# Performance work log

Measured on AMD Instinct MI355X. Metric: run time of the kernel, lower is better.

## Reference

```python
import jax, jax.numpy as jnp
import numpy as np

D_MODEL = 1024
NUM_HEADS = 16
HEAD_DIM = D_MODEL // NUM_HEADS
BATCH, SEQ = 2, 2048


def setup_inputs() -> dict:
    key = jax.random.key(0)
    ks = jax.random.split(key, 11)
    s = 1.0 / np.sqrt(D_MODEL)
    inp = {
        "query": jax.random.normal(ks[0], (BATCH, SEQ, D_MODEL), jnp.float32),
        "key": jax.random.normal(ks[1], (BATCH, SEQ, D_MODEL), jnp.float32),
        "value": jax.random.normal(ks[2], (BATCH, SEQ, D_MODEL), jnp.float32),
        "q_w": jax.random.uniform(ks[3], (D_MODEL, D_MODEL), jnp.float32, -s, s),
        "q_b": jax.random.uniform(ks[4], (D_MODEL,), jnp.float32, -s, s),
        "k_w": jax.random.uniform(ks[5], (D_MODEL, D_MODEL), jnp.float32, -s, s),
        "k_b": jax.random.uniform(ks[6], (D_MODEL,), jnp.float32, -s, s),
        "v_w": jax.random.uniform(ks[7], (D_MODEL, D_MODEL), jnp.float32, -s, s),
        "v_b": jax.random.uniform(ks[8], (D_MODEL,), jnp.float32, -s, s),
        "o_w": jax.random.uniform(ks[9], (D_MODEL, D_MODEL), jnp.float32, -s, s),
        "o_b": jax.random.uniform(ks[10], (D_MODEL,), jnp.float32, -s, s),
    }
    return inp


def reference(query, key, value, q_w, q_b, k_w, k_b, v_w, v_b, o_w, o_b):
    B = query.shape[0]
    # linear projections (torch Linear: x @ W^T + b)
    q = query @ q_w.T + q_b
    k = key @ k_w.T + k_b
    v = value @ v_w.T + v_b
    # split heads: [B, S, D] -> [B, H, S, Hd]
    def split(x):
        return x.reshape(B, -1, NUM_HEADS, HEAD_DIM).transpose(0, 2, 1, 3)
    q, k, v = split(q), split(k), split(v)
    scores = jnp.einsum("bhqd,bhkd->bhqk", q, k) / np.sqrt(HEAD_DIM).astype(np.float32)
    attn = jax.nn.softmax(scores, axis=-1)
    out = jnp.einsum("bhqk,bhkd->bhqd", attn, v)  # [B,H,S,Hd]
    merged = out.transpose(0, 2, 1, 3).reshape(B, -1, D_MODEL)
    return merged @ o_w.T + o_b
```

## Files before the change

kernel.cpp:

```cpp
#include <hip/hip_runtime.h>
#include <hip/hip_bf16.h>

typedef unsigned short u16;
typedef unsigned int u32;
typedef __attribute__((ext_vector_type(8))) short short8;
typedef __attribute__((ext_vector_type(4))) short s16x4;
typedef __attribute__((ext_vector_type(4))) float f32x4;

__device__ __forceinline__ u16 f2bf(float f) {
    u32 u = __float_as_uint(f);
    return (u16)((u + 0x7FFFu + ((u >> 16) & 1u)) >> 16);
}
__device__ __forceinline__ u32 pack2bf(float a, float b) {
    __hip_bfloat162 h = __float22bfloat162_rn(float2{a, b});
    return *reinterpret_cast<u32*>(&h);
}

#if __has_builtin(__builtin_amdgcn_exp2f)
#define EXP2(x) __builtin_amdgcn_exp2f(x)
#else
#define EXP2(x) exp2f(x)
#endif

__device__ __forceinline__ void gload16(const void* g, void* s) {
    __builtin_amdgcn_global_load_lds(
        (const __attribute__((address_space(1))) void*)g,
        (__attribute__((address_space(3))) void*)s, 16, 0, 0);
}

__global__ __launch_bounds__(256) void cast_all_kernel(
    const float* __restrict__ s0, const float* __restrict__ s1, const float* __restrict__ s2,
    const float* __restrict__ s3, const float* __restrict__ s4, const float* __restrict__ s5,
    const float* __restrict__ s6,
    u16* __restrict__ d0, u16* __restrict__ d1, u16* __restrict__ d2,
    u16* __restrict__ d3, u16* __restrict__ d4, u16* __restrict__ d5,
    u16* __restrict__ d6, int nBig, int nSmall)
{
    const int y = blockIdx.y;
    const float* s = y == 0 ? s0 : (y == 1 ? s1 : (y == 2 ? s2 : (y == 3 ? s3 : (y == 4 ? s4 : (y == 5 ? s5 : s6)))));
    u16* d = y == 0 ? d0 : (y == 1 ? d1 : (y == 2 ? d2 : (y == 3 ? d3 : (y == 4 ? d4 : (y == 5 ? d5 : d6)))));
    const int n = (y < 3) ? nBig : nSmall;
    int i = (blockIdx.x * 256 + threadIdx.x) * 4;
    const int stride = gridDim.x * 256 * 4;
    for (; i < n; i += stride) {
        float4 v = *(const float4*)(s + i);
        uint2 t;
        t.x = pack2bf(v.x, v.y);
        t.y = pack2bf(v.z, v.w);
        *(uint2*)(d + i) = t;
    }
}

__global__ __launch_bounds__(256) void qkv_gemm(
    const u16* __restrict__ Xq, const u16* __restrict__ Xk, const u16* __restrict__ Xv,
    const u16* __restrict__ Wq, const u16* __restrict__ Wk, const u16* __restrict__ Wv,
    const float* __restrict__ qb, const float* __restrict__ kb, const float* __restrict__ vb,
    u16* __restrict__ Qo, u16* __restrict__ Ko, u16* __restrict__ Vo)
{
    constexpr int N = 1024, K = 1024;
    __shared__ __align__(16) u16 Asm[128 * 32];
    __shared__ __align__(16) u16 Bsm[128 * 32];
    const int z = blockIdx.z;
    const u16* A = z == 0 ? Xq : (z == 1 ? Xk : Xv);
    const u16* W = z == 0 ? Wq : (z == 1 ? Wk : Wv);
    const float* bias = z == 0 ? qb : (z == 1 ? kb : vb);

    const int tid = threadIdx.x;
    const int wid = tid >> 6;
    const int lane = tid & 63;
    const int r15 = lane & 15, g = lane >> 4;
    const int m0 = blockIdx.y * 128, n0 = blockIdx.x * 128;
    const int wr = wid >> 1, wc = wid & 1;

    f32x4 acc[4][4];
#pragma unroll
    for (int i = 0; i < 4; ++i)
#pragma unroll
        for (int j = 0; j < 4; ++j) acc[i][j] = (f32x4){0.f, 0.f, 0.f, 0.f};

    const int idx0 = tid, idx1 = tid + 256;
    const size_t aoff0 = (size_t)(m0 + (idx0 >> 2)) * K + (idx0 & 3) * 8;
    const size_t aoff1 = (size_t)(m0 + (idx1 >> 2)) * K + (idx1 & 3) * 8;
    const size_t boff0 = (size_t)(n0 + (idx0 >> 2)) * K + (idx0 & 3) * 8;
    const size_t boff1 = (size_t)(n0 + (idx1 >> 2)) * K + (idx1 & 3) * 8;
    u16* dA0 = Asm + wid * 512;
    u16* dA1 = Asm + 2048 + wid * 512;
    u16* dB0 = Bsm + wid * 512;
    u16* dB1 = Bsm + 2048 + wid * 512;

    for (int kt = 0; kt < K; kt += 32) {
        gload16(A + aoff0 + kt, dA0);
        gload16(A + aoff1 + kt, dA1);
        gload16(W + boff0 + kt, dB0);
        gload16(W + boff1 + kt, dB1);
        __syncthreads();
        short8 af[4], bfr[4];
#pragma unroll
        for (int i = 0; i < 4; ++i) {
            af[i]  = *(const short8*)(Asm + (wr * 64 + i * 16 + r15) * 32 + g * 8);
            bfr[i] = *(const short8*)(Bsm + (wc * 64 + i * 16 + r15) * 32 + g * 8);
        }
#pragma unroll
        for (int i = 0; i < 4; ++i)
#pragma unroll
            for (int j = 0; j < 4; ++j)
                acc[i][j] = __builtin_amdgcn_mfma_f32_16x16x32_bf16(af[i], bfr[j], acc[i][j], 0, 0, 0);
        __syncthreads();
    }

    const float scale = (z == 0) ? 0.125f * 1.4426950408889634f : 1.0f;
    u16* ob = z == 0 ? Qo : (z == 1 ? Ko : Vo);
#pragma unroll
    for (int i = 0; i < 4; ++i) {
        const int mbase = m0 + wr * 64 + i * 16 + g * 4;
#pragma unroll
        for (int j = 0; j < 4; ++j) {
            const int n = n0 + wc * 64 + j * 16 + r15;
            const float bb = bias[n];
            if (z < 2) {
#pragma unroll
                for (int r = 0; r < 4; ++r)
                    ob[(size_t)(mbase + r) * N + n] = f2bf((acc[i][j][r] + bb) * scale);
            } else {
                const int b_ = mbase >> 11, s_ = mbase & 2047;
                s16x4 pk;
#pragma unroll
                for (int r = 0; r < 4; ++r) pk[r] = (short)f2bf(acc[i][j][r] + bb);
                *(s16x4*)(ob + ((size_t)b_ << 21) + (size_t)n * 2048 + s_) = pk;
            }
        }
    }
}

__global__ __launch_bounds__(256) void o_gemm(
    const u16* __restrict__ A, const u16* __restrict__ W,
    const float* __restrict__ bias, float* __restrict__ outp)
{
    constexpr int N = 1024, K = 1024;
    __shared__ __align__(16) u16 Asm[128 * 32];
    __shared__ __align__(16) u16 Bsm[128 * 32];
    const int tid = threadIdx.x;
    const int wid = tid >> 6;
    const int lane = tid & 63;
    const int r15 = lane & 15, g = lane >> 4;
    const int m0 = blockIdx.y * 128, n0 = blockIdx.x * 128;
    const int wr = wid >> 1, wc = wid & 1;

    f32x4 acc[4][4];
#pragma unroll
    for (int i = 0; i < 4; ++i)
#pragma unroll
        for (int j = 0; j < 4; ++j) acc[i][j] = (f32x4){0.f, 0.f, 0.f, 0.f};

    const int idx0 = tid, idx1 = tid + 256;
    const size_t aoff0 = (size_t)(m0 + (idx0 >> 2)) * K + (idx0 & 3) * 8;
    const size_t aoff1 = (size_t)(m0 + (idx1 >> 2)) * K + (idx1 & 3) * 8;
    const size_t boff0 = (size_t)(n0 + (idx0 >> 2)) * K + (idx0 & 3) * 8;
    const size_t boff1 = (size_t)(n0 + (idx1 >> 2)) * K + (idx1 & 3) * 8;
    u16* dA0 = Asm + wid * 512;
    u16* dA1 = Asm + 2048 + wid * 512;
    u16* dB0 = Bsm + wid * 512;
    u16* dB1 = Bsm + 2048 + wid * 512;

    for (int kt = 0; kt < K; kt += 32) {
        gload16(A + aoff0 + kt, dA0);
        gload16(A + aoff1 + kt, dA1);
        gload16(W + boff0 + kt, dB0);
        gload16(W + boff1 + kt, dB1);
        __syncthreads();
        short8 af[4], bfr[4];
#pragma unroll
        for (int i = 0; i < 4; ++i) {
            af[i]  = *(const short8*)(Asm + (wr * 64 + i * 16 + r15) * 32 + g * 8);
            bfr[i] = *(const short8*)(Bsm + (wc * 64 + i * 16 + r15) * 32 + g * 8);
        }
#pragma unroll
        for (int i = 0; i < 4; ++i)
#pragma unroll
            for (int j = 0; j < 4; ++j)
                acc[i][j] = __builtin_amdgcn_mfma_f32_16x16x32_bf16(af[i], bfr[j], acc[i][j], 0, 0, 0);
        __syncthreads();
    }

#pragma unroll
    for (int i = 0; i < 4; ++i) {
        const int mbase = m0 + wr * 64 + i * 16 + g * 4;
#pragma unroll
        for (int j = 0; j < 4; ++j) {
            const int n = n0 + wc * 64 + j * 16 + r15;
            const float bb = bias[n];
#pragma unroll
            for (int r = 0; r < 4; ++r)
                outp[(size_t)(mbase + r) * N + n] = acc[i][j][r] + bb;
        }
    }
}

__global__ __launch_bounds__(256) void attn_kernel(
    const u16* __restrict__ Q, const u16* __restrict__ Kb,
    const u16* __restrict__ Vt, u16* __restrict__ Mo)
{
    __shared__ __align__(16) u16 Ksm[32 * 64];
    __shared__ __align__(16) u16 Vsm[64 * 32];
    __shared__ __align__(16) u16 Psm[4 * 16 * 40];
    const int tid = threadIdx.x;
    const int wid = tid >> 6, lane = tid & 63;
    const int r15 = lane & 15, g = lane >> 4;
    const int b = blockIdx.y >> 4, h = blockIdx.y & 15;
    const int q0 = blockIdx.x * 64 + wid * 16;

    const u16* Qrow = Q + ((size_t)b * 2048 + q0 + r15) * 1024 + h * 64;
    short8 qf[2];
    qf[0] = *(const short8*)(Qrow + g * 8);
    qf[1] = *(const short8*)(Qrow + 32 + g * 8);

    const int krow = tid >> 3;
    const int kslot = (tid & 7) ^ (krow & 7);
    const u16* Ksrc = Kb + ((size_t)b * 2048 + krow) * 1024 + h * 64 + kslot * 8;
    const int vrow = tid >> 2;
    const int vslot = (tid & 3) ^ (vrow & 3);
    const u16* Vsrc = Vt + ((size_t)b << 21) + (size_t)(h * 64 + vrow) * 2048 + vslot * 8;
    u16* kdst = Ksm + wid * 512;
    u16* vdst = Vsm + wid * 512;

    f32x4 acc[4];
#pragma unroll
    for (int d = 0; d < 4; ++d) acc[d] = (f32x4){0.f, 0.f, 0.f, 0.f};
    float lsum = 0.f;
    u16* Pw = Psm + wid * 640;

    for (int k0 = 0; k0 < 2048; k0 += 32) {
        __syncthreads();
        gload16(Ksrc + (size_t)k0 * 1024, kdst);
        gload16(Vsrc + k0, vdst);
        __syncthreads();

        short8 kf[2][2];
#pragma unroll
        for (int t = 0; t < 2; ++t)
#pragma unroll
            for (int f = 0; f < 2; ++f) {
                const int row = t * 16 + r15;
                kf[t][f] = *(const short8*)(Ksm + row * 64 + (((f * 4 + g) ^ (row & 7)) * 8));
            }

        f32x4 st0 = (f32x4){0.f, 0.f, 0.f, 0.f};
        f32x4 st1 = (f32x4){0.f, 0.f, 0.f, 0.f};
        st0 = __builtin_amdgcn_mfma_f32_16x16x32_bf16(kf[0][0], qf[0], st0, 0, 0, 0);
        st0 = __builtin_amdgcn_mfma_f32_16x16x32_bf16(kf[0][1], qf[1], st0, 0, 0, 0);
        st1 = __builtin_amdgcn_mfma_f32_16x16x32_bf16(kf[1][0], qf[0], st1, 0, 0, 0);
        st1 = __builtin_amdgcn_mfma_f32_16x16x32_bf16(kf[1][1], qf[1], st1, 0, 0, 0);

        float p[8];
#pragma unroll
        for (int r = 0; r < 4; ++r) { p[r] = EXP2(st0[r]); p[4 + r] = EXP2(st1[r]); }
        float ps = ((p[0] + p[1]) + (p[2] + p[3])) + ((p[4] + p[5]) + (p[6] + p[7]));
        ps += __shfl_xor(ps, 16, 64);
        ps += __shfl_xor(ps, 32, 64);
        lsum += ps;

        uint2 pk0, pk1;
        pk0.x = pack2bf(p[0], p[1]); pk0.y = pack2bf(p[2], p[3]);
        pk1.x = pack2bf(p[4], p[5]); pk1.y = pack2bf(p[6], p[7]);
        *(uint2*)(Pw + r15 * 40 + 4 * g) = pk0;
        *(uint2*)(Pw + r15 * 40 + 16 + 4 * g) = pk1;

        short8 pf = *(const short8*)(Pw + r15 * 40 + g * 8);

#pragma unroll
        for (int d = 0; d < 4; ++d) {
            const int row = d * 16 + r15;
            short8 vf = *(const short8*)(Vsm + row * 32 + ((g ^ (row & 3)) * 8));
            acc[d] = __builtin_amdgcn_mfma_f32_16x16x32_bf16(vf, pf, acc[d], 0, 0, 0);
        }
    }

    const float inv = 1.f / lsum;
    const size_t orow = ((size_t)b * 2048 + q0 + r15) * 1024 + h * 64;
#pragma unroll
    for (int d = 0; d < 4; ++d) {
        uint2 pk;
        pk.x = pack2bf(acc[d][0] * inv, acc[d][1] * inv);
        pk.y = pack2bf(acc[d][2] * inv, acc[d][3] * inv);
        *(uint2*)(Mo + orow + d * 16 + g * 4) = pk;
    }
}

extern "C" void kernel_launch(void* const* d_in, const int* in_sizes, int n_in,
                              void* d_out, int out_size, void* d_ws, size_t ws_size,
                              hipStream_t stream) {
    (void)in_sizes; (void)n_in; (void)out_size; (void)ws_size;
    const float* query = (const float*)d_in[0];
    const float* key   = (const float*)d_in[1];
    const float* value = (const float*)d_in[2];
    const float* q_w = (const float*)d_in[3];
    const float* q_b = (const float*)d_in[4];
    const float* k_w = (const float*)d_in[5];
    const float* k_b = (const float*)d_in[6];
    const float* v_w = (const float*)d_in[7];
    const float* v_b = (const float*)d_in[8];
    const float* o_w = (const float*)d_in[9];
    const float* o_b = (const float*)d_in[10];

    const size_t NE = (size_t)4096 * 1024;
    const size_t MW = (size_t)1024 * 1024;
    u16* w = (u16*)d_ws;
    u16* Xq = w;
    u16* Xk = Xq + NE;
    u16* Xv = Xk + NE;
    u16* Wq = Xv + NE;
    u16* Wk = Wq + MW;
    u16* Wv = Wk + MW;
    u16* Wo = Wv + MW;
    u16* Qb = Wo + MW;
    u16* Kb = Qb + NE;
    u16* Vt = Kb + NE;
    u16* Mo = Vt + NE;

    cast_all_kernel<<<dim3(2048, 7), 256, 0, stream>>>(
        query, key, value, q_w, k_w, v_w, o_w,
        Xq, Xk, Xv, Wq, Wk, Wv, Wo, (int)NE, (int)MW);
    qkv_gemm<<<dim3(8, 32, 3), 256, 0, stream>>>(
        Xq, Xk, Xv, Wq, Wk, Wv, q_b, k_b, v_b, Qb, Kb, Vt);
    attn_kernel<<<dim3(32, 32), 256, 0, stream>>>(Qb, Kb, Vt, Mo);
    o_gemm<<<dim3(8, 32), 256, 0, stream>>>(Mo, Wo, o_b, (float*)d_out);
}
```

Baseline: 166.4 us.

## Double-buffer GEMM and attention tiles, remap blocks, and keep P in registers

Both projection GEMMs and the attention kernel now double-buffer their LDS tiles, so the load of the next K-step is issued before the current step is computed. The GEMM and attention kernels also remap block indices so that neighbouring blocks reuse cached data. The attention kernel now gives each warp 32 queries and each block a 64-key tile, uses half as many blocks, and permutes the V-transpose storage so that exp(P) packed in registers feeds the MFMA B operand directly with no LDS round-trip. The row-sum reduction is deferred to the end of the kernel. The changes raise LDS use and register pressure, and they depend on the V-layout permutation and the loop barriers being correct.

```diff
diff --git a/kernel.cpp b/kernel.cpp
--- a/kernel.cpp
+++ b/kernel.cpp
@@ -6,6 +6,7 @@
 typedef __attribute__((ext_vector_type(8))) short short8;
 typedef __attribute__((ext_vector_type(4))) short s16x4;
 typedef __attribute__((ext_vector_type(4))) float f32x4;
+typedef __attribute__((ext_vector_type(4))) u32 u32v4;
 
 __device__ __forceinline__ u16 f2bf(float f) {
     u32 u = __float_as_uint(f);
@@ -58,8 +59,8 @@
     u16* __restrict__ Qo, u16* __restrict__ Ko, u16* __restrict__ Vo)
 {
     constexpr int N = 1024, K = 1024;
-    __shared__ __align__(16) u16 Asm[128 * 32];
-    __shared__ __align__(16) u16 Bsm[128 * 32];
+    __shared__ __align__(16) u16 Asm[2][4096];
+    __shared__ __align__(16) u16 Bsm[2][4096];
     const int z = blockIdx.z;
     const u16* A = z == 0 ? Xq : (z == 1 ? Xk : Xv);
     const u16* W = z == 0 ? Wq : (z == 1 ? Wk : Wv);
@@ -69,7 +70,9 @@
     const int wid = tid >> 6;
     const int lane = tid & 63;
     const int r15 = lane & 15, g = lane >> 4;
-    const int m0 = blockIdx.y * 128, n0 = blockIdx.x * 128;
+    const int fb = blockIdx.y * 8 + blockIdx.x;
+    const int lsw = (fb & 7) * 32 + (fb >> 3);
+    const int m0 = (lsw >> 3) * 128, n0 = (lsw & 7) * 128;
     const int wr = wid >> 1, wc = wid & 1;
 
     f32x4 acc[4][4];
@@ -83,22 +86,24 @@
     const size_t aoff1 = (size_t)(m0 + (idx1 >> 2)) * K + (idx1 & 3) * 8;
     const size_t boff0 = (size_t)(n0 + (idx0 >> 2)) * K + (idx0 & 3) * 8;
     const size_t boff1 = (size_t)(n0 + (idx1 >> 2)) * K + (idx1 & 3) * 8;
-    u16* dA0 = Asm + wid * 512;
-    u16* dA1 = Asm + 2048 + wid * 512;
-    u16* dB0 = Bsm + wid * 512;
-    u16* dB1 = Bsm + 2048 + wid * 512;
-
-    for (int kt = 0; kt < K; kt += 32) {
-        gload16(A + aoff0 + kt, dA0);
-        gload16(A + aoff1 + kt, dA1);
-        gload16(W + boff0 + kt, dB0);
-        gload16(W + boff1 + kt, dB1);
-        __syncthreads();
+
+    auto STAGE = [&](int buf, int kt) {
+        gload16(A + aoff0 + kt, &Asm[buf][wid * 512]);
+        gload16(A + aoff1 + kt, &Asm[buf][2048 + wid * 512]);
+        gload16(W + boff0 + kt, &Bsm[buf][wid * 512]);
+        gload16(W + boff1 + kt, &Bsm[buf][2048 + wid * 512]);
+    };
+
+    STAGE(0, 0);
+    __syncthreads();
+    for (int t = 0; t < 32; ++t) {
+        const int buf = t & 1;
+        if (t < 31) STAGE(buf ^ 1, (t + 1) * 32);
         short8 af[4], bfr[4];
 #pragma unroll
         for (int i = 0; i < 4; ++i) {
-            af[i]  = *(const short8*)(Asm + (wr * 64 + i * 16 + r15) * 32 + g * 8);
-            bfr[i] = *(const short8*)(Bsm + (wc * 64 + i * 16 + r15) * 32 + g * 8);
+            af[i]  = *(const short8*)(&Asm[buf][0] + (wr * 64 + i * 16 + r15) * 32 + g * 8);
+            bfr[i] = *(const short8*)(&Bsm[buf][0] + (wc * 64 + i * 16 + r15) * 32 + g * 8);
         }
 #pragma unroll
         for (int i = 0; i < 4; ++i)
@@ -123,10 +128,13 @@
                     ob[(size_t)(mbase + r) * N + n] = f2bf((acc[i][j][r] + bb) * scale);
             } else {
                 const int b_ = mbase >> 11, s_ = mbase & 2047;
+                const int blk = (s_ >> 2) & 7;
+                const int pb = ((blk & 3) << 1) | (blk >> 2);
+                const int s_new = (s_ & ~31) | (pb << 2);
                 s16x4 pk;
 #pragma unroll
                 for (int r = 0; r < 4; ++r) pk[r] = (short)f2bf(acc[i][j][r] + bb);
-                *(s16x4*)(ob + ((size_t)b_ << 21) + (size_t)n * 2048 + s_) = pk;
+                *(s16x4*)(ob + ((size_t)b_ << 21) + (size_t)n * 2048 + s_new) = pk;
             }
         }
     }
@@ -137,13 +145,15 @@
     const float* __restrict__ bias, float* __restrict__ outp)
 {
     constexpr int N = 1024, K = 1024;
-    __shared__ __align__(16) u16 Asm[128 * 32];
-    __shared__ __align__(16) u16 Bsm[128 * 32];
+    __shared__ __align__(16) u16 Asm[2][4096];
+    __shared__ __align__(16) u16 Bsm[2][4096];
     const int tid = threadIdx.x;
     const int wid = tid >> 6;
     const int lane = tid & 63;
     const int r15 = lane & 15, g = lane >> 4;
-    const int m0 = blockIdx.y * 128, n0 = blockIdx.x * 128;
+    const int fb = blockIdx.y * 8 + blockIdx.x;
+    const int lsw = (fb & 7) * 32 + (fb >> 3);
+    const int m0 = (lsw >> 3) * 128, n0 = (lsw & 7) * 128;
     const int wr = wid >> 1, wc = wid & 1;
 
     f32x4 acc[4][4];
@@ -157,22 +167,24 @@
     const size_t aoff1 = (size_t)(m0 + (idx1 >> 2)) * K + (idx1 & 3) * 8;
     const size_t boff0 = (size_t)(n0 + (idx0 >> 2)) * K + (idx0 & 3) * 8;
     const size_t boff1 = (size_t)(n0 + (idx1 >> 2)) * K + (idx1 & 3) * 8;
-    u16* dA0 = Asm + wid * 512;
-    u16* dA1 = Asm + 2048 + wid * 512;
-    u16* dB0 = Bsm + wid * 512;
-    u16* dB1 = Bsm + 2048 + wid * 512;
-
-    for (int kt = 0; kt < K; kt += 32) {
-        gload16(A + aoff0 + kt, dA0);
-        gload16(A + aoff1 + kt, dA1);
-        gload16(W + boff0 + kt, dB0);
-        gload16(W + boff1 + kt, dB1);
-        __syncthreads();
+
+    auto STAGE = [&](int buf, int kt) {
+        gload16(A + aoff0 + kt, &Asm[buf][wid * 512]);
+        gload16(A + aoff1 + kt, &Asm[buf][2048 + wid * 512]);
+        gload16(W + boff0 + kt, &Bsm[buf][wid * 512]);
+        gload16(W + boff1 + kt, &Bsm[buf][2048 + wid * 512]);
+    };
+
+    STAGE(0, 0);
+    __syncthreads();
+    for (int t = 0; t < 32; ++t) {
+        const int buf = t & 1;
+        if (t < 31) STAGE(buf ^ 1, (t + 1) * 32);
         short8 af[4], bfr[4];
 #pragma unroll
         for (int i = 0; i < 4; ++i) {
-            af[i]  = *(const short8*)(Asm + (wr * 64 + i * 16 + r15) * 32 + g * 8);
-            bfr[i] = *(const short8*)(Bsm + (wc * 64 + i * 16 + r15) * 32 + g * 8);
+            af[i]  = *(const short8*)(&Asm[buf][0] + (wr * 64 + i * 16 + r15) * 32 + g * 8);
+            bfr[i] = *(const short8*)(&Bsm[buf][0] + (wc * 64 + i * 16 + r15) * 32 + g * 8);
         }
 #pragma unroll
         for (int i = 0; i < 4; ++i)
@@ -200,89 +212,120 @@
     const u16* __restrict__ Q, const u16* __restrict__ Kb,
     const u16* __restrict__ Vt, u16* __restrict__ Mo)
 {
-    __shared__ __align__(16) u16 Ksm[32 * 64];
-    __shared__ __align__(16) u16 Vsm[64 * 32];
-    __shared__ __align__(16) u16 Psm[4 * 16 * 40];
+    __shared__ __align__(16) u16 Ksm[2][4096];
+    __shared__ __align__(16) u16 Vsm[2][4096];
     const int tid = threadIdx.x;
     const int wid = tid >> 6, lane = tid & 63;
     const int r15 = lane & 15, g = lane >> 4;
-    const int b = blockIdx.y >> 4, h = blockIdx.y & 15;
-    const int q0 = blockIdx.x * 64 + wid * 16;
-
-    const u16* Qrow = Q + ((size_t)b * 2048 + q0 + r15) * 1024 + h * 64;
-    short8 qf[2];
-    qf[0] = *(const short8*)(Qrow + g * 8);
-    qf[1] = *(const short8*)(Qrow + 32 + g * 8);
-
-    const int krow = tid >> 3;
-    const int kslot = (tid & 7) ^ (krow & 7);
-    const u16* Ksrc = Kb + ((size_t)b * 2048 + krow) * 1024 + h * 64 + kslot * 8;
-    const int vrow = tid >> 2;
-    const int vslot = (tid & 3) ^ (vrow & 3);
-    const u16* Vsrc = Vt + ((size_t)b << 21) + (size_t)(h * 64 + vrow) * 2048 + vslot * 8;
-    u16* kdst = Ksm + wid * 512;
-    u16* vdst = Vsm + wid * 512;
-
-    f32x4 acc[4];
-#pragma unroll
-    for (int d = 0; d < 4; ++d) acc[d] = (f32x4){0.f, 0.f, 0.f, 0.f};
-    float lsum = 0.f;
-    u16* Pw = Psm + wid * 640;
-
-    for (int k0 = 0; k0 < 2048; k0 += 32) {
+    const int bid = blockIdx.x;
+    const int l = (bid & 7) * 64 + (bid >> 3);
+    const int bh = l >> 4;
+    const int b = bh >> 4, h = bh & 15;
+    const int q0 = (l & 15) * 128 + wid * 32;
+
+    const u16* Qbase = Q + ((size_t)b * 2048 + q0) * 1024 + h * 64;
+    short8 qf[2][2];
+#pragma unroll
+    for (int qt = 0; qt < 2; ++qt)
+#pragma unroll
+        for (int f = 0; f < 2; ++f)
+            qf[qt][f] = *(const short8*)(Qbase + (size_t)(qt * 16 + r15) * 1024 + f * 32 + g * 8);
+
+    const int p0 = tid, p1 = tid + 256;
+    const int row0 = p0 >> 3, slot0 = (p0 & 7) ^ (row0 & 7);
+    const int row1 = p1 >> 3, slot1 = (p1 & 7) ^ (row1 & 7);
+    const u16* Ks0 = Kb + ((size_t)b * 2048 + row0) * 1024 + h * 64 + slot0 * 8;
+    const u16* Ks1 = Kb + ((size_t)b * 2048 + row1) * 1024 + h * 64 + slot1 * 8;
+    const u16* Vs0 = Vt + ((size_t)b << 21) + (size_t)(h * 64 + row0) * 2048 + slot0 * 8;
+    const u16* Vs1 = Vt + ((size_t)b << 21) + (size_t)(h * 64 + row1) * 2048 + slot1 * 8;
+
+    f32x4 acc[2][4];
+#pragma unroll
+    for (int qt = 0; qt < 2; ++qt)
+#pragma unroll
+        for (int d4 = 0; d4 < 4; ++d4) acc[qt][d4] = (f32x4){0.f, 0.f, 0.f, 0.f};
+    float lsum[2] = {0.f, 0.f};
+
+    auto STAGE = [&](int buf, int k0) {
+        gload16(Ks0 + (size_t)k0 * 1024, &Ksm[buf][wid * 512]);
+        gload16(Ks1 + (size_t)k0 * 1024, &Ksm[buf][2048 + wid * 512]);
+        gload16(Vs0 + k0, &Vsm[buf][wid * 512]);
+        gload16(Vs1 + k0, &Vsm[buf][2048 + wid * 512]);
+    };
+
+    STAGE(0, 0);
+    __syncthreads();
+
+    const int sA = r15 & 7;
+    for (int t = 0; t < 32; ++t) {
+        const int buf = t & 1;
+        if (t < 31) STAGE(buf ^ 1, (t + 1) * 64);
+
+        const u16* Kp = &Ksm[buf][0];
+        const u16* Vp = &Vsm[buf][0];
+        short8 kf[4][2];
+#pragma unroll
+        for (int kt = 0; kt < 4; ++kt)
+#pragma unroll
+            for (int f = 0; f < 2; ++f)
+                kf[kt][f] = *(const short8*)(Kp + (kt * 16 + r15) * 64 + (((f * 4 + g) ^ sA) * 8));
+
+        f32x4 st[2][4];
+#pragma unroll
+        for (int qt = 0; qt < 2; ++qt)
+#pragma unroll
+            for (int kt = 0; kt < 4; ++kt) {
+                f32x4 zz = (f32x4){0.f, 0.f, 0.f, 0.f};
+                zz = __builtin_amdgcn_mfma_f32_16x16x32_bf16(kf[kt][0], qf[qt][0], zz, 0, 0, 0);
+                zz = __builtin_amdgcn_mfma_f32_16x16x32_bf16(kf[kt][1], qf[qt][1], zz, 0, 0, 0);
+                st[qt][kt] = zz;
+            }
+
+        u32 pk[2][8];
+#pragma unroll
+        for (int qt = 0; qt < 2; ++qt) {
+            float s = 0.f;
+#pragma unroll
+            for (int kt = 0; kt < 4; ++kt) {
+                float e0 = EXP2(st[qt][kt][0]);
+                float e1 = EXP2(st[qt][kt][1]);
+                float e2 = EXP2(st[qt][kt][2]);
+                float e3 = EXP2(st[qt][kt][3]);
+                s += (e0 + e1) + (e2 + e3);
+                pk[qt][kt * 2]     = pack2bf(e0, e1);
+                pk[qt][kt * 2 + 1] = pack2bf(e2, e3);
+            }
+            lsum[qt] += s;
+        }
+
+#pragma unroll
+        for (int d4 = 0; d4 < 4; ++d4) {
+#pragma unroll
+            for (int kk = 0; kk < 2; ++kk) {
+                short8 vf = *(const short8*)(Vp + (d4 * 16 + r15) * 64 + (((kk * 4 + g) ^ sA) * 8));
+                u32v4 b0 = {pk[0][kk * 4], pk[0][kk * 4 + 1], pk[0][kk * 4 + 2], pk[0][kk * 4 + 3]};
+                u32v4 b1 = {pk[1][kk * 4], pk[1][kk * 4 + 1], pk[1][kk * 4 + 2], pk[1][kk * 4 + 3]};
+                acc[0][d4] = __builtin_amdgcn_mfma_f32_16x16x32_bf16(vf, __builtin_bit_cast(short8, b0), acc[0][d4], 0, 0, 0);
+                acc[1][d4] = __builtin_amdgcn_mfma_f32_16x16x32_bf16(vf, __builtin_bit_cast(short8, b1), acc[1][d4], 0, 0, 0);
+            }
+        }
         __syncthreads();
-        gload16(Ksrc + (size_t)k0 * 1024, kdst);
-        gload16(Vsrc + k0, vdst);
-        __syncthreads();
-
-        short8 kf[2][2];
-#pragma unroll
-        for (int t = 0; t < 2; ++t)
-#pragma unroll
-            for (int f = 0; f < 2; ++f) {
-                const int row = t * 16 + r15;
-                kf[t][f] = *(const short8*)(Ksm + row * 64 + (((f * 4 + g) ^ (row & 7)) * 8));
-            }
-
-        f32x4 st0 = (f32x4){0.f, 0.f, 0.f, 0.f};
-        f32x4 st1 = (f32x4){0.f, 0.f, 0.f, 0.f};
-        st0 = __builtin_amdgcn_mfma_f32_16x16x32_bf16(kf[0][0], qf[0], st0, 0, 0, 0);
-        st0 = __builtin_amdgcn_mfma_f32_16x16x32_bf16(kf[0][1], qf[1], st0, 0, 0, 0);
-        st1 = __builtin_amdgcn_mfma_f32_16x16x32_bf16(kf[1][0], qf[0], st1, 0, 0, 0);
-        st1 = __builtin_amdgcn_mfma_f32_16x16x32_bf16(kf[1][1], qf[1], st1, 0, 0, 0);
-
-        float p[8];
-#pragma unroll
-        for (int r = 0; r < 4; ++r) { p[r] = EXP2(st0[r]); p[4 + r] = EXP2(st1[r]); }
-        float ps = ((p[0] + p[1]) + (p[2] + p[3])) + ((p[4] + p[5]) + (p[6] + p[7]));
-        ps += __shfl_xor(ps, 16, 64);
-        ps += __shfl_xor(ps, 32, 64);
-        lsum += ps;
-
-        uint2 pk0, pk1;
-        pk0.x = pack2bf(p[0], p[1]); pk0.y = pack2bf(p[2], p[3]);
-        pk1.x = pack2bf(p[4], p[5]); pk1.y = pack2bf(p[6], p[7]);
-        *(uint2*)(Pw + r15 * 40 + 4 * g) = pk0;
-        *(uint2*)(Pw + r15 * 40 + 16 + 4 * g) = pk1;
-
-        short8 pf = *(const short8*)(Pw + r15 * 40 + g * 8);
-
-#pragma unroll
-        for (int d = 0; d < 4; ++d) {
-            const int row = d * 16 + r15;
-            short8 vf = *(const short8*)(Vsm + row * 32 + ((g ^ (row & 3)) * 8));
-            acc[d] = __builtin_amdgcn_mfma_f32_16x16x32_bf16(vf, pf, acc[d], 0, 0, 0);
-        }
-    }
-
-    const float inv = 1.f / lsum;
-    const size_t orow = ((size_t)b * 2048 + q0 + r15) * 1024 + h * 64;
-#pragma unroll
-    for (int d = 0; d < 4; ++d) {
-        uint2 pk;
-        pk.x = pack2bf(acc[d][0] * inv, acc[d][1] * inv);
-        pk.y = pack2bf(acc[d][2] * inv, acc[d][3] * inv);
-        *(uint2*)(Mo + orow + d * 16 + g * 4) = pk;
+    }
+
+#pragma unroll
+    for (int qt = 0; qt < 2; ++qt) {
+        float ls = lsum[qt];
+        ls += __shfl_xor(ls, 16, 64);
+        ls += __shfl_xor(ls, 32, 64);
+        const float inv = 1.f / ls;
+        const size_t orow = ((size_t)b * 2048 + q0 + qt * 16 + r15) * 1024 + h * 64;
+#pragma unroll
+        for (int d4 = 0; d4 < 4; ++d4) {
+            uint2 o;
+            o.x = pack2bf(acc[qt][d4][0] * inv, acc[qt][d4][1] * inv);
+            o.y = pack2bf(acc[qt][d4][2] * inv, acc[qt][d4][3] * inv);
+            *(uint2*)(Mo + orow + d4 * 16 + g * 4) = o;
+        }
     }
 }
 
@@ -322,6 +365,6 @@
         Xq, Xk, Xv, Wq, Wk, Wv, Wo, (int)NE, (int)MW);
     qkv_gemm<<<dim3(8, 32, 3), 256, 0, stream>>>(
         Xq, Xk, Xv, Wq, Wk, Wv, q_b, k_b, v_b, Qb, Kb, Vt);
-    attn_kernel<<<dim3(32, 32), 256, 0, stream>>>(Qb, Kb, Vt, Mo);
+    attn_kernel<<<dim3(512), 256, 0, stream>>>(Qb, Kb, Vt, Mo);
     o_gemm<<<dim3(8, 32), 256, 0, stream>>>(Mo, Wo, o_b, (float*)d_out);
 }
```

Result: faster. 142.7 us (-14.2%).
